# Kernel tuning notes

Hardware: AMD Instinct MI355X
Metric: run time of the kernel (lower is better)

The kernel has to match this reference:

```python
import jax, jax.numpy as jnp
import numpy as np

B, T, I, H, C = 64, 2048, 128, 256, 64


def setup_inputs() -> dict:
    key = jax.random.key(0)
    ks = jax.random.split(key, 12)
    s_ih = 1.0 / np.sqrt(H)
    inp = {
        "x": jax.random.normal(ks[0], (B, T, I), dtype=jnp.float32),
        # layer 0 GRU params (PyTorch layout: W_ih [3H, I], W_hh [3H, H])
        "W_ih0": jax.random.uniform(ks[1], (3 * H, I), minval=-s_ih, maxval=s_ih, dtype=jnp.float32),
        "W_hh0": jax.random.uniform(ks[2], (3 * H, H), minval=-s_ih, maxval=s_ih, dtype=jnp.float32),
        "b_ih0": jax.random.uniform(ks[3], (3 * H,), minval=-s_ih, maxval=s_ih, dtype=jnp.float32),
        "b_hh0": jax.random.uniform(ks[4], (3 * H,), minval=-s_ih, maxval=s_ih, dtype=jnp.float32),
        # layer 1 GRU params (input is H)
        "W_ih1": jax.random.uniform(ks[5], (3 * H, H), minval=-s_ih, maxval=s_ih, dtype=jnp.float32),
        "W_hh1": jax.random.uniform(ks[6], (3 * H, H), minval=-s_ih, maxval=s_ih, dtype=jnp.float32),
        "b_ih1": jax.random.uniform(ks[7], (3 * H,), minval=-s_ih, maxval=s_ih, dtype=jnp.float32),
        "b_hh1": jax.random.uniform(ks[8], (3 * H,), minval=-s_ih, maxval=s_ih, dtype=jnp.float32),
        # classifier head
        "fc_w": jax.random.uniform(ks[9], (C, H), minval=-s_ih, maxval=s_ih, dtype=jnp.float32),
        "fc_b": jax.random.uniform(ks[10], (C,), minval=-s_ih, maxval=s_ih, dtype=jnp.float32),
    }
    return inp


def _gru_layer(inp, W_ih, W_hh, b_ih, b_hh):
    # inp: [B, T, D_in] -> out: [B, T, H]; PyTorch GRU cell math.
    h_dim = W_hh.shape[1]
    # Precompute input-side gate pre-activations for the whole sequence (one big GEMM).
    gates_x = jnp.einsum("btd,gd->btg", inp, W_ih) + b_ih  # [B, T, 3H]

    def step(h, gx):
        gh = h @ W_hh.T + b_hh  # [B, 3H]
        xr, xz, xn = jnp.split(gx, 3, axis=-1)
        hr, hz, hn = jnp.split(gh, 3, axis=-1)
        r = jax.nn.sigmoid(xr + hr)
        z = jax.nn.sigmoid(xz + hz)
        n = jnp.tanh(xn + r * hn)
        h_new = (1.0 - z) * n + z * h
        return h_new, h_new

    h0 = jnp.zeros((inp.shape[0], h_dim), dtype=inp.dtype)
    _, out_tbh = jax.lax.scan(step, h0, jnp.swapaxes(gates_x, 0, 1))  # [T, B, H]
    return jnp.swapaxes(out_tbh, 0, 1)  # [B, T, H]


def reference(x, W_ih0, W_hh0, b_ih0, b_hh0, W_ih1, W_hh1, b_ih1, b_hh1, fc_w, fc_b):
    h = _gru_layer(x, W_ih0, W_hh0, b_ih0, b_hh0)
    h = _gru_layer(h, W_ih1, W_hh1, b_ih1, b_hh1)
    return h @ fc_w.T + fc_b  # [B, T, C]
```

## Files before the change

### kernel.cpp

```cpp
#include <hip/hip_runtime.h>

typedef _Float16 half2_t __attribute__((ext_vector_type(2)));
typedef _Float16 half8_t __attribute__((ext_vector_type(8)));
typedef float floatx4 __attribute__((ext_vector_type(4)));
typedef unsigned int u32;

#define BB 64
#define TT 2048
#define II 128
#define HH 256
#define CC 64
#define G3 (3*HH)
#define MTOT (BB*TT)

static __device__ __forceinline__ float dot2f(half2_t a, half2_t b, float c) {
#if __has_builtin(__builtin_amdgcn_fdot2)
    return __builtin_amdgcn_fdot2(a, b, c, false);
#else
    return c + (float)a[0]*(float)b[0] + (float)a[1]*(float)b[1];
#endif
}

template<typename AT, typename CT>
__global__ __launch_bounds__(256, 2)
void gemm_mfma(const AT* __restrict__ A, const float* __restrict__ W,
               const float* __restrict__ bias, CT* __restrict__ Cout,
               int M, int N, int K)
{
    __shared__ alignas(16) u32 As32[128 * 32];
    __shared__ alignas(16) u32 Bs32[64 * 32];

    const int tid  = threadIdx.x;
    const int lane = tid & 63;
    const int wave = tid >> 6;
    const int wm   = wave >> 1;
    const int wn   = wave & 1;
    const int m0   = blockIdx.y * 128;
    const int n0   = blockIdx.x * 64;
    const int lr   = lane & 15;
    const int lg   = lane >> 4;

    floatx4 acc[4][2] = {};

    for (int kc = 0; kc < K; kc += 64) {
        #pragma unroll
        for (int it = 0; it < 4; ++it) {
            const int s    = it * 256 + tid;
            const int row  = s >> 3;
            const int slot = s & 7;
            const AT* src  = A + (size_t)(m0 + row) * K + kc + slot * 8;
            half8_t v;
            if constexpr (sizeof(AT) == 2) {
                v = *reinterpret_cast<const half8_t*>(src);
            } else {
                const float4* s4 = reinterpret_cast<const float4*>(src);
                float4 lo = s4[0], hi = s4[1];
                v[0] = (_Float16)lo.x; v[1] = (_Float16)lo.y;
                v[2] = (_Float16)lo.z; v[3] = (_Float16)lo.w;
                v[4] = (_Float16)hi.x; v[5] = (_Float16)hi.y;
                v[6] = (_Float16)hi.z; v[7] = (_Float16)hi.w;
            }
            const int sw = slot ^ (row & 7);
            *reinterpret_cast<half8_t*>(&As32[row * 32 + sw * 4]) = v;
        }
        #pragma unroll
        for (int it = 0; it < 2; ++it) {
            const int s    = it * 256 + tid;
            const int row  = s >> 3;
            const int slot = s & 7;
            const float* src = W + (size_t)(n0 + row) * K + kc + slot * 8;
            const float4* s4 = reinterpret_cast<const float4*>(src);
            float4 lo = s4[0], hi = s4[1];
            half8_t v;
            v[0] = (_Float16)lo.x; v[1] = (_Float16)lo.y;
            v[2] = (_Float16)lo.z; v[3] = (_Float16)lo.w;
            v[4] = (_Float16)hi.x; v[5] = (_Float16)hi.y;
            v[6] = (_Float16)hi.z; v[7] = (_Float16)hi.w;
            const int sw = slot ^ (row & 7);
            *reinterpret_cast<half8_t*>(&Bs32[row * 32 + sw * 4]) = v;
        }
        __syncthreads();

        #pragma unroll
        for (int ks = 0; ks < 2; ++ks) {
            half8_t af[4], bf[2];
            #pragma unroll
            for (int fm = 0; fm < 4; ++fm) {
                const int row  = wm * 64 + fm * 16 + lr;
                const int slot = ks * 4 + lg;
                const int sw   = slot ^ (row & 7);
                af[fm] = *reinterpret_cast<const half8_t*>(&As32[row * 32 + sw * 4]);
            }
            #pragma unroll
            for (int fn = 0; fn < 2; ++fn) {
                const int row  = wn * 32 + fn * 16 + lr;
                const int slot = ks * 4 + lg;
                const int sw   = slot ^ (row & 7);
                bf[fn] = *reinterpret_cast<const half8_t*>(&Bs32[row * 32 + sw * 4]);
            }
            #pragma unroll
            for (int fm = 0; fm < 4; ++fm)
                #pragma unroll
                for (int fn = 0; fn < 2; ++fn)
                    acc[fm][fn] = __builtin_amdgcn_mfma_f32_16x16x32_f16(
                        af[fm], bf[fn], acc[fm][fn], 0, 0, 0);
        }
        __syncthreads();
    }

    #pragma unroll
    for (int fn = 0; fn < 2; ++fn) {
        const int n = n0 + wn * 32 + fn * 16 + lr;
        const float bv = bias[n];
        #pragma unroll
        for (int fm = 0; fm < 4; ++fm) {
            #pragma unroll
            for (int r = 0; r < 4; ++r) {
                const int m = m0 + wm * 64 + fm * 16 + lg * 4 + r;
                Cout[(size_t)m * N + n] = (CT)(acc[fm][fn][r] + bv);
            }
        }
    }
}

__global__ __launch_bounds__(512, 2)
void gru_scan(const _Float16* __restrict__ gx,
              const float* __restrict__ Whh,
              const float* __restrict__ bhh,
              _Float16* __restrict__ hout)
{
    const int b  = blockIdx.x;
    const int t  = threadIdx.x;
    const int j  = t >> 1;
    const int kh = t & 1;

    half2_t w0[64], w1[64], w2[64];
    {
        const float* p0 = Whh + (size_t)j * HH + kh * 128;
        const float* p1 = p0 + 256 * HH;
        const float* p2 = p0 + 512 * HH;
        #pragma unroll
        for (int i = 0; i < 64; ++i) {
            w0[i] = half2_t{(_Float16)p0[2*i], (_Float16)p0[2*i+1]};
            w1[i] = half2_t{(_Float16)p1[2*i], (_Float16)p1[2*i+1]};
            w2[i] = half2_t{(_Float16)p2[2*i], (_Float16)p2[2*i+1]};
        }
    }
    const float bh_r = bhh[j], bh_z = bhh[HH + j], bh_n = bhh[2*HH + j];

    __shared__ alignas(16) u32 h2[HH/2];
    if (t < HH/2) h2[t] = 0u;
    float hprev = 0.f;
    __syncthreads();

    const _Float16* g = gx + (size_t)b * TT * G3;
    u32* op = (u32*)(hout + (size_t)b * TT * HH);

    for (int step = 0; step < TT; ++step) {
        float xr = (float)g[j];
        float xz = (float)g[HH + j];
        float xn = (float)g[2*HH + j];

        const uint4* hb = (const uint4*)(h2 + kh * 64);
        float ar = 0.f, az = 0.f, an = 0.f;
        #pragma unroll
        for (int c = 0; c < 16; ++c) {
            uint4 hv = hb[c];
            half2_t ha = __builtin_bit_cast(half2_t, hv.x);
            half2_t hc = __builtin_bit_cast(half2_t, hv.y);
            half2_t hd = __builtin_bit_cast(half2_t, hv.z);
            half2_t he = __builtin_bit_cast(half2_t, hv.w);
            ar = dot2f(ha, w0[4*c+0], ar); az = dot2f(ha, w1[4*c+0], az); an = dot2f(ha, w2[4*c+0], an);
            ar = dot2f(hc, w0[4*c+1], ar); az = dot2f(hc, w1[4*c+1], az); an = dot2f(hc, w2[4*c+1], an);
            ar = dot2f(hd, w0[4*c+2], ar); az = dot2f(hd, w1[4*c+2], az); an = dot2f(hd, w2[4*c+2], an);
            ar = dot2f(he, w0[4*c+3], ar); az = dot2f(he, w1[4*c+3], az); an = dot2f(he, w2[4*c+3], an);
        }
        ar += __shfl_xor(ar, 1);
        az += __shfl_xor(az, 1);
        an += __shfl_xor(an, 1);

        const float r = 1.f / (1.f + __expf(-(xr + ar + bh_r)));
        const float z = 1.f / (1.f + __expf(-(xz + az + bh_z)));
        const float e = __expf(2.f * (xn + r * (an + bh_n)));
        const float n = 1.f - 2.f / (e + 1.f);
        const float hnew = (1.f - z) * n + z * hprev;
        hprev = hnew;

        const float hother = __shfl_xor(hnew, 2);
        __syncthreads();
        if ((t & 3) == 0) {
            half2_t hp{(_Float16)hnew, (_Float16)hother};
            const u32 pu = __builtin_bit_cast(u32, hp);
            h2[t >> 2] = pu;
            op[t >> 2] = pu;
        }
        __syncthreads();
        g  += G3;
        op += HH/2;
    }
}

extern "C" void kernel_launch(void* const* d_in, const int* in_sizes, int n_in,
                              void* d_out, int out_size, void* d_ws, size_t ws_size,
                              hipStream_t stream) {
    const float* x    = (const float*)d_in[0];
    const float* Wih0 = (const float*)d_in[1];
    const float* Whh0 = (const float*)d_in[2];
    const float* bih0 = (const float*)d_in[3];
    const float* bhh0 = (const float*)d_in[4];
    const float* Wih1 = (const float*)d_in[5];
    const float* Whh1 = (const float*)d_in[6];
    const float* bih1 = (const float*)d_in[7];
    const float* bhh1 = (const float*)d_in[8];
    const float* fcw  = (const float*)d_in[9];
    const float* fcb  = (const float*)d_in[10];
    float* out = (float*)d_out;

    _Float16* gxbuf = (_Float16*)d_ws;
    _Float16* hbuf  = (_Float16*)((char*)d_ws + (size_t)MTOT * G3 * sizeof(_Float16));

    const dim3 blk(256);
    gemm_mfma<float, _Float16><<<dim3(G3/64, MTOT/128), blk, 0, stream>>>(
        x, Wih0, bih0, gxbuf, MTOT, G3, II);
    gru_scan<<<dim3(BB), dim3(512), 0, stream>>>(gxbuf, Whh0, bhh0, hbuf);
    gemm_mfma<_Float16, _Float16><<<dim3(G3/64, MTOT/128), blk, 0, stream>>>(
        hbuf, Wih1, bih1, gxbuf, MTOT, G3, HH);
    gru_scan<<<dim3(BB), dim3(512), 0, stream>>>(gxbuf, Whh1, bhh1, hbuf);
    gemm_mfma<_Float16, float><<<dim3(CC/64, MTOT/128), blk, 0, stream>>>(
        hbuf, fcw, fcb, out, MTOT, CC, HH);
}
```

Measured before the change: 5.213 ms.

## Split GRU scan K across 4 lanes, double-buffer hidden state, prefetch gates

The recurrent scan now runs 1024 threads per batch with each hidden unit's dot product split across four lanes instead of two. This halves per-thread weight registers and the serial dot-product chain, with the partial sums reduced by DPP quad moves. The hidden state is double-buffered in shared memory, so each step needs one barrier instead of two. Next-step gate inputs are prefetched, and divisions become hardware reciprocals. The costs are more threads per block, a slightly less accurate reciprocal, and 16-bit scattered stores to output and shared memory.

```diff
diff --git a/kernel.cpp b/kernel.cpp
--- a/kernel.cpp
+++ b/kernel.cpp
@@ -19,6 +19,23 @@
 #else
     return c + (float)a[0]*(float)b[0] + (float)a[1]*(float)b[1];
 #endif
+}
+
+static __device__ __forceinline__ half2_t bch2(u32 x) {
+    return __builtin_bit_cast(half2_t, x);
+}
+
+static __device__ __forceinline__ float quad_allsum(float x) {
+    int i = __builtin_bit_cast(int, x);
+    int a = __builtin_amdgcn_mov_dpp(i, 0xB1, 0xF, 0xF, true);
+    float y = x + __builtin_bit_cast(float, a);
+    int k = __builtin_bit_cast(int, y);
+    int b = __builtin_amdgcn_mov_dpp(k, 0x4E, 0xF, 0xF, true);
+    return y + __builtin_bit_cast(float, b);
+}
+
+static __device__ __forceinline__ float fast_rcp(float x) {
+    return __builtin_amdgcn_rcpf(x);
 }
 
 template<typename AT, typename CT>
@@ -123,7 +140,7 @@
     }
 }
 
-__global__ __launch_bounds__(512, 2)
+__global__ __launch_bounds__(1024, 4)
 void gru_scan(const _Float16* __restrict__ gx,
               const float* __restrict__ Whh,
               const float* __restrict__ bhh,
@@ -131,16 +148,16 @@
 {
     const int b  = blockIdx.x;
     const int t  = threadIdx.x;
-    const int j  = t >> 1;
-    const int kh = t & 1;
-
-    half2_t w0[64], w1[64], w2[64];
+    const int j  = t >> 2;
+    const int kq = t & 3;
+
+    half2_t w0[32], w1[32], w2[32];
     {
-        const float* p0 = Whh + (size_t)j * HH + kh * 128;
+        const float* p0 = Whh + (size_t)j * HH + kq * 64;
         const float* p1 = p0 + 256 * HH;
         const float* p2 = p0 + 512 * HH;
         #pragma unroll
-        for (int i = 0; i < 64; ++i) {
+        for (int i = 0; i < 32; ++i) {
             w0[i] = half2_t{(_Float16)p0[2*i], (_Float16)p0[2*i+1]};
             w1[i] = half2_t{(_Float16)p1[2*i], (_Float16)p1[2*i+1]};
             w2[i] = half2_t{(_Float16)p2[2*i], (_Float16)p2[2*i+1]};
@@ -148,55 +165,55 @@
     }
     const float bh_r = bhh[j], bh_z = bhh[HH + j], bh_n = bhh[2*HH + j];
 
-    __shared__ alignas(16) u32 h2[HH/2];
-    if (t < HH/2) h2[t] = 0u;
+    __shared__ alignas(16) _Float16 hs[2][HH];
+    if (t < HH/2) reinterpret_cast<u32*>(hs[0])[t] = 0u;
     float hprev = 0.f;
+
+    const _Float16* gj = gx + (size_t)b * TT * G3 + j;
+    _Float16* op = hout + (size_t)b * TT * HH + j;
+
+    float xr = (float)gj[0];
+    float xz = (float)gj[HH];
+    float xn = (float)gj[2*HH];
     __syncthreads();
 
-    const _Float16* g = gx + (size_t)b * TT * G3;
-    u32* op = (u32*)(hout + (size_t)b * TT * HH);
-
     for (int step = 0; step < TT; ++step) {
-        float xr = (float)g[j];
-        float xz = (float)g[HH + j];
-        float xn = (float)g[2*HH + j];
-
-        const uint4* hb = (const uint4*)(h2 + kh * 64);
+        const _Float16* gn = gj + G3;
+        const _Float16 pxr = gn[0];
+        const _Float16 pxz = gn[HH];
+        const _Float16 pxn = gn[2*HH];
+
+        const uint4* hb = reinterpret_cast<const uint4*>(hs[step & 1] + kq * 64);
         float ar = 0.f, az = 0.f, an = 0.f;
         #pragma unroll
-        for (int c = 0; c < 16; ++c) {
-            uint4 hv = hb[c];
-            half2_t ha = __builtin_bit_cast(half2_t, hv.x);
-            half2_t hc = __builtin_bit_cast(half2_t, hv.y);
-            half2_t hd = __builtin_bit_cast(half2_t, hv.z);
-            half2_t he = __builtin_bit_cast(half2_t, hv.w);
+        for (int c = 0; c < 8; ++c) {
+            const uint4 hv = hb[c];
+            const half2_t ha = bch2(hv.x), hc = bch2(hv.y);
+            const half2_t hd = bch2(hv.z), he = bch2(hv.w);
             ar = dot2f(ha, w0[4*c+0], ar); az = dot2f(ha, w1[4*c+0], az); an = dot2f(ha, w2[4*c+0], an);
             ar = dot2f(hc, w0[4*c+1], ar); az = dot2f(hc, w1[4*c+1], az); an = dot2f(hc, w2[4*c+1], an);
             ar = dot2f(hd, w0[4*c+2], ar); az = dot2f(hd, w1[4*c+2], az); an = dot2f(hd, w2[4*c+2], an);
             ar = dot2f(he, w0[4*c+3], ar); az = dot2f(he, w1[4*c+3], az); an = dot2f(he, w2[4*c+3], an);
         }
-        ar += __shfl_xor(ar, 1);
-        az += __shfl_xor(az, 1);
-        an += __shfl_xor(an, 1);
-
-        const float r = 1.f / (1.f + __expf(-(xr + ar + bh_r)));
-        const float z = 1.f / (1.f + __expf(-(xz + az + bh_z)));
+        ar = quad_allsum(ar);
+        az = quad_allsum(az);
+        an = quad_allsum(an);
+
+        const float r = fast_rcp(1.f + __expf(-(xr + ar + bh_r)));
+        const float z = fast_rcp(1.f + __expf(-(xz + az + bh_z)));
         const float e = __expf(2.f * (xn + r * (an + bh_n)));
-        const float n = 1.f - 2.f / (e + 1.f);
-        const float hnew = (1.f - z) * n + z * hprev;
+        const float nn = 1.f - 2.f * fast_rcp(e + 1.f);
+        const float hnew = (1.f - z) * nn + z * hprev;
         hprev = hnew;
 
-        const float hother = __shfl_xor(hnew, 2);
+        if (kq == 0) {
+            hs[(step + 1) & 1][j] = (_Float16)hnew;
+            op[0] = (_Float16)hnew;
+        }
         __syncthreads();
-        if ((t & 3) == 0) {
-            half2_t hp{(_Float16)hnew, (_Float16)hother};
-            const u32 pu = __builtin_bit_cast(u32, hp);
-            h2[t >> 2] = pu;
-            op[t >> 2] = pu;
-        }
-        __syncthreads();
-        g  += G3;
-        op += HH/2;
+
+        gj = gn; op += HH;
+        xr = (float)pxr; xz = (float)pxz; xn = (float)pxn;
     }
 }
 
@@ -222,10 +239,10 @@
     const dim3 blk(256);
     gemm_mfma<float, _Float16><<<dim3(G3/64, MTOT/128), blk, 0, stream>>>(
         x, Wih0, bih0, gxbuf, MTOT, G3, II);
-    gru_scan<<<dim3(BB), dim3(512), 0, stream>>>(gxbuf, Whh0, bhh0, hbuf);
+    gru_scan<<<dim3(BB), dim3(1024), 0, stream>>>(gxbuf, Whh0, bhh0, hbuf);
     gemm_mfma<_Float16, _Float16><<<dim3(G3/64, MTOT/128), blk, 0, stream>>>(
         hbuf, Wih1, bih1, gxbuf, MTOT, G3, HH);
-    gru_scan<<<dim3(BB), dim3(512), 0, stream>>>(gxbuf, Whh1, bhh1, hbuf);
+    gru_scan<<<dim3(BB), dim3(1024), 0, stream>>>(gxbuf, Whh1, bhh1, hbuf);
     gemm_mfma<_Float16, float><<<dim3(CC/64, MTOT/128), blk, 0, stream>>>(
         hbuf, fcw, fcb, out, MTOT, CC, HH);
 }
```

Result: faster. 5.106 ms (-2.0%).

## Compute GRU recurrent matvec with MFMA and double-buffer hidden state in LDS

Applied to the files above, without the earlier changes.

The recurrent h·W_hh product in the scan kernel now runs on 16x16x32 f16 MFMA instructions, with h broadcast across the A rows and W_hh fragments held in registers. Previously it used per-thread fdot2 loops with a pair-shuffle reduction. The hidden state is double-buffered in LDS so each step needs one barrier instead of two. The next step's gate inputs are prefetched, and sigmoid/tanh use a hardware reciprocal. The trade-off is that 15 of 16 MFMA rows are wasted, only 16 lanes per wave do the gate math, and 48 half8 weight fragments per thread raise register pressure.

```diff
diff --git a/kernel.cpp b/kernel.cpp
--- a/kernel.cpp
+++ b/kernel.cpp
@@ -13,12 +13,8 @@
 #define G3 (3*HH)
 #define MTOT (BB*TT)
 
-static __device__ __forceinline__ float dot2f(half2_t a, half2_t b, float c) {
-#if __has_builtin(__builtin_amdgcn_fdot2)
-    return __builtin_amdgcn_fdot2(a, b, c, false);
-#else
-    return c + (float)a[0]*(float)b[0] + (float)a[1]*(float)b[1];
-#endif
+static __device__ __forceinline__ float fast_rcp(float x) {
+    return __builtin_amdgcn_rcpf(x);
 }
 
 template<typename AT, typename CT>
@@ -129,74 +125,106 @@
               const float* __restrict__ bhh,
               _Float16* __restrict__ hout)
 {
-    const int b  = blockIdx.x;
-    const int t  = threadIdx.x;
-    const int j  = t >> 1;
-    const int kh = t & 1;
-
-    half2_t w0[64], w1[64], w2[64];
-    {
-        const float* p0 = Whh + (size_t)j * HH + kh * 128;
-        const float* p1 = p0 + 256 * HH;
-        const float* p2 = p0 + 512 * HH;
-        #pragma unroll
-        for (int i = 0; i < 64; ++i) {
-            w0[i] = half2_t{(_Float16)p0[2*i], (_Float16)p0[2*i+1]};
-            w1[i] = half2_t{(_Float16)p1[2*i], (_Float16)p1[2*i+1]};
-            w2[i] = half2_t{(_Float16)p2[2*i], (_Float16)p2[2*i+1]};
-        }
-    }
-    const float bh_r = bhh[j], bh_z = bhh[HH + j], bh_n = bhh[2*HH + j];
-
-    __shared__ alignas(16) u32 h2[HH/2];
-    if (t < HH/2) h2[t] = 0u;
-    float hprev = 0.f;
+    const int b    = blockIdx.x;
+    const int tid  = threadIdx.x;
+    const int wv   = tid >> 6;
+    const int lane = tid & 63;
+    const int lr   = lane & 15;
+    const int lg   = lane >> 4;
+
+    half8_t wf[48];
+    #pragma unroll
+    for (int g = 0; g < 3; ++g) {
+        #pragma unroll
+        for (int p = 0; p < 2; ++p) {
+            const int row = g * 256 + wv * 32 + p * 16 + lr;
+            #pragma unroll
+            for (int kf = 0; kf < 8; ++kf) {
+                const float* src = Whh + (size_t)row * HH + kf * 32 + lg * 8;
+                const float4 lo = reinterpret_cast<const float4*>(src)[0];
+                const float4 hi = reinterpret_cast<const float4*>(src)[1];
+                half8_t v;
+                v[0] = (_Float16)lo.x; v[1] = (_Float16)lo.y;
+                v[2] = (_Float16)lo.z; v[3] = (_Float16)lo.w;
+                v[4] = (_Float16)hi.x; v[5] = (_Float16)hi.y;
+                v[6] = (_Float16)hi.z; v[7] = (_Float16)hi.w;
+                wf[(g * 2 + p) * 8 + kf] = v;
+            }
+        }
+    }
+
+    const int j0 = wv * 32 + lr;
+    float bhr[2], bhz[2], bhn[2];
+    #pragma unroll
+    for (int p = 0; p < 2; ++p) {
+        bhr[p] = bhh[j0 + p * 16];
+        bhz[p] = bhh[HH + j0 + p * 16];
+        bhn[p] = bhh[2 * HH + j0 + p * 16];
+    }
+
+    __shared__ alignas(16) _Float16 Hs[2][HH];
+    reinterpret_cast<_Float16*>(Hs)[tid] = (_Float16)0.f;
+
+    const _Float16* gp = gx + (size_t)b * TT * G3 + j0;
+    _Float16* op = hout + (size_t)b * TT * HH + j0;
+
+    _Float16 pxr0 = 0, pxz0 = 0, pxn0 = 0, pxr1 = 0, pxz1 = 0, pxn1 = 0;
+    if (lane < 16) {
+        pxr0 = gp[0];       pxr1 = gp[16];
+        pxz0 = gp[HH];      pxz1 = gp[HH + 16];
+        pxn0 = gp[2 * HH];  pxn1 = gp[2 * HH + 16];
+    }
+    float hp0 = 0.f, hp1 = 0.f;
     __syncthreads();
 
-    const _Float16* g = gx + (size_t)b * TT * G3;
-    u32* op = (u32*)(hout + (size_t)b * TT * HH);
-
-    for (int step = 0; step < TT; ++step) {
-        float xr = (float)g[j];
-        float xz = (float)g[HH + j];
-        float xn = (float)g[2*HH + j];
-
-        const uint4* hb = (const uint4*)(h2 + kh * 64);
-        float ar = 0.f, az = 0.f, an = 0.f;
-        #pragma unroll
-        for (int c = 0; c < 16; ++c) {
-            uint4 hv = hb[c];
-            half2_t ha = __builtin_bit_cast(half2_t, hv.x);
-            half2_t hc = __builtin_bit_cast(half2_t, hv.y);
-            half2_t hd = __builtin_bit_cast(half2_t, hv.z);
-            half2_t he = __builtin_bit_cast(half2_t, hv.w);
-            ar = dot2f(ha, w0[4*c+0], ar); az = dot2f(ha, w1[4*c+0], az); an = dot2f(ha, w2[4*c+0], an);
-            ar = dot2f(hc, w0[4*c+1], ar); az = dot2f(hc, w1[4*c+1], az); an = dot2f(hc, w2[4*c+1], an);
-            ar = dot2f(hd, w0[4*c+2], ar); az = dot2f(hd, w1[4*c+2], az); an = dot2f(hd, w2[4*c+2], an);
-            ar = dot2f(he, w0[4*c+3], ar); az = dot2f(he, w1[4*c+3], az); an = dot2f(he, w2[4*c+3], an);
-        }
-        ar += __shfl_xor(ar, 1);
-        az += __shfl_xor(az, 1);
-        an += __shfl_xor(an, 1);
-
-        const float r = 1.f / (1.f + __expf(-(xr + ar + bh_r)));
-        const float z = 1.f / (1.f + __expf(-(xz + az + bh_z)));
-        const float e = __expf(2.f * (xn + r * (an + bh_n)));
-        const float n = 1.f - 2.f / (e + 1.f);
-        const float hnew = (1.f - z) * n + z * hprev;
-        hprev = hnew;
-
-        const float hother = __shfl_xor(hnew, 2);
+    for (int t = 0; t < TT; ++t) {
+        const _Float16* hcur = Hs[t & 1];
+        _Float16*       hnxt = Hs[(t + 1) & 1];
+
+        floatx4 acc[6] = {};
+        #pragma unroll
+        for (int kf = 0; kf < 8; ++kf) {
+            const half8_t a = *reinterpret_cast<const half8_t*>(&hcur[kf * 32 + lg * 8]);
+            #pragma unroll
+            for (int i = 0; i < 6; ++i)
+                acc[i] = __builtin_amdgcn_mfma_f32_16x16x32_f16(
+                    a, wf[i * 8 + kf], acc[i], 0, 0, 0);
+        }
+
+        if (lane < 16) {
+            const _Float16 nxr0 = gp[G3],           nxr1 = gp[G3 + 16];
+            const _Float16 nxz0 = gp[G3 + HH],      nxz1 = gp[G3 + HH + 16];
+            const _Float16 nxn0 = gp[G3 + 2 * HH],  nxn1 = gp[G3 + 2 * HH + 16];
+
+            {
+                const float ar = acc[0][0], az = acc[2][0], an = acc[4][0];
+                const float r = fast_rcp(1.f + __expf(-((float)pxr0 + ar + bhr[0])));
+                const float z = fast_rcp(1.f + __expf(-((float)pxz0 + az + bhz[0])));
+                const float e = __expf(2.f * ((float)pxn0 + r * (an + bhn[0])));
+                const float n = 1.f - 2.f * fast_rcp(e + 1.f);
+                const float hnew = (1.f - z) * n + z * hp0;
+                hp0 = hnew;
+                const _Float16 hf = (_Float16)hnew;
+                hnxt[j0] = hf;
+                op[0] = hf;
+            }
+            {
+                const float ar = acc[1][0], az = acc[3][0], an = acc[5][0];
+                const float r = fast_rcp(1.f + __expf(-((float)pxr1 + ar + bhr[1])));
+                const float z = fast_rcp(1.f + __expf(-((float)pxz1 + az + bhz[1])));
+                const float e = __expf(2.f * ((float)pxn1 + r * (an + bhn[1])));
+                const float n = 1.f - 2.f * fast_rcp(e + 1.f);
+                const float hnew = (1.f - z) * n + z * hp1;
+                hp1 = hnew;
+                const _Float16 hf = (_Float16)hnew;
+                hnxt[j0 + 16] = hf;
+                op[16] = hf;
+            }
+            pxr0 = nxr0; pxz0 = nxz0; pxn0 = nxn0;
+            pxr1 = nxr1; pxz1 = nxz1; pxn1 = nxn1;
+        }
         __syncthreads();
-        if ((t & 3) == 0) {
-            half2_t hp{(_Float16)hnew, (_Float16)hother};
-            const u32 pu = __builtin_bit_cast(u32, hp);
-            h2[t >> 2] = pu;
-            op[t >> 2] = pu;
-        }
-        __syncthreads();
-        g  += G3;
-        op += HH/2;
+        gp += G3; op += HH;
     }
 }
 
```

Result: slower. 5.415 ms (+3.9%).

## Double-buffer GRU hidden state, prefetch gate inputs, use DPP lane exchange

Applied to the files above, without the earlier changes.

The GRU recurrence kernel now ping-pongs the shared hidden state between two buffers. This lets each timestep use a single barrier instead of two. It also loads the next timestep's input-gate values one step ahead, so their global latency overlaps the current step's dot products. Lane exchanges switch from shuffle to DPP moves and the divisions in the gates use the hardware reciprocal, both to shorten the per-step serial critical path. The prefetch reads one row past the end of each batch's gate buffer on the last step, and the reciprocal is slightly less precise than a true division.

```diff
diff --git a/kernel.cpp b/kernel.cpp
--- a/kernel.cpp
+++ b/kernel.cpp
@@ -19,6 +19,25 @@
 #else
     return c + (float)a[0]*(float)b[0] + (float)a[1]*(float)b[1];
 #endif
+}
+
+static __device__ __forceinline__ half2_t bch2(u32 x) {
+    return __builtin_bit_cast(half2_t, x);
+}
+
+static __device__ __forceinline__ float fast_rcp(float x) {
+    return __builtin_amdgcn_rcpf(x);
+}
+
+static __device__ __forceinline__ float pair_sum(float x) {
+    int i = __builtin_bit_cast(int, x);
+    int a = __builtin_amdgcn_mov_dpp(i, 0xB1, 0xF, 0xF, true);
+    return x + __builtin_bit_cast(float, a);
+}
+static __device__ __forceinline__ float dpp_xor2(float x) {
+    int i = __builtin_bit_cast(int, x);
+    int a = __builtin_amdgcn_mov_dpp(i, 0x4E, 0xF, 0xF, true);
+    return __builtin_bit_cast(float, a);
 }
 
 template<typename AT, typename CT>
@@ -123,7 +142,8 @@
     }
 }
 
-__global__ __launch_bounds__(512, 2)
+__global__ __attribute__((amdgpu_flat_work_group_size(512, 512),
+                          amdgpu_waves_per_eu(2, 2)))
 void gru_scan(const _Float16* __restrict__ gx,
               const float* __restrict__ Whh,
               const float* __restrict__ bhh,
@@ -136,67 +156,68 @@
 
     half2_t w0[64], w1[64], w2[64];
     {
-        const float* p0 = Whh + (size_t)j * HH + kh * 128;
-        const float* p1 = p0 + 256 * HH;
-        const float* p2 = p0 + 512 * HH;
+        const float2* q0 = reinterpret_cast<const float2*>(Whh + (size_t)j * HH + kh * 128);
+        const float2* q1 = q0 + 128 * HH;
+        const float2* q2 = q0 + 256 * HH;
         #pragma unroll
         for (int i = 0; i < 64; ++i) {
-            w0[i] = half2_t{(_Float16)p0[2*i], (_Float16)p0[2*i+1]};
-            w1[i] = half2_t{(_Float16)p1[2*i], (_Float16)p1[2*i+1]};
-            w2[i] = half2_t{(_Float16)p2[2*i], (_Float16)p2[2*i+1]};
+            const float2 a = q0[i], c = q1[i], d = q2[i];
+            w0[i] = half2_t{(_Float16)a.x, (_Float16)a.y};
+            w1[i] = half2_t{(_Float16)c.x, (_Float16)c.y};
+            w2[i] = half2_t{(_Float16)d.x, (_Float16)d.y};
         }
     }
     const float bh_r = bhh[j], bh_z = bhh[HH + j], bh_n = bhh[2*HH + j];
 
-    __shared__ alignas(16) u32 h2[HH/2];
-    if (t < HH/2) h2[t] = 0u;
+    __shared__ alignas(16) _Float16 Hs[2][HH];
+    reinterpret_cast<_Float16*>(Hs)[t] = (_Float16)0.f;
     float hprev = 0.f;
+
+    const _Float16* gp = gx + (size_t)b * TT * G3 + j;
+    u32* opw = (u32*)(hout + (size_t)b * TT * HH);
+
+    _Float16 pxr = gp[0], pxz = gp[HH], pxn = gp[2*HH];
     __syncthreads();
 
-    const _Float16* g = gx + (size_t)b * TT * G3;
-    u32* op = (u32*)(hout + (size_t)b * TT * HH);
-
     for (int step = 0; step < TT; ++step) {
-        float xr = (float)g[j];
-        float xz = (float)g[HH + j];
-        float xn = (float)g[2*HH + j];
-
-        const uint4* hb = (const uint4*)(h2 + kh * 64);
+        const _Float16 nxr = gp[G3];
+        const _Float16 nxz = gp[G3 + HH];
+        const _Float16 nxn = gp[G3 + 2*HH];
+
+        const uint4* hb = reinterpret_cast<const uint4*>(Hs[step & 1] + kh * 128);
         float ar = 0.f, az = 0.f, an = 0.f;
         #pragma unroll
         for (int c = 0; c < 16; ++c) {
-            uint4 hv = hb[c];
-            half2_t ha = __builtin_bit_cast(half2_t, hv.x);
-            half2_t hc = __builtin_bit_cast(half2_t, hv.y);
-            half2_t hd = __builtin_bit_cast(half2_t, hv.z);
-            half2_t he = __builtin_bit_cast(half2_t, hv.w);
+            const uint4 hv = hb[c];
+            const half2_t ha = bch2(hv.x), hc = bch2(hv.y);
+            const half2_t hd = bch2(hv.z), he = bch2(hv.w);
             ar = dot2f(ha, w0[4*c+0], ar); az = dot2f(ha, w1[4*c+0], az); an = dot2f(ha, w2[4*c+0], an);
             ar = dot2f(hc, w0[4*c+1], ar); az = dot2f(hc, w1[4*c+1], az); an = dot2f(hc, w2[4*c+1], an);
             ar = dot2f(hd, w0[4*c+2], ar); az = dot2f(hd, w1[4*c+2], az); an = dot2f(hd, w2[4*c+2], an);
             ar = dot2f(he, w0[4*c+3], ar); az = dot2f(he, w1[4*c+3], az); an = dot2f(he, w2[4*c+3], an);
         }
-        ar += __shfl_xor(ar, 1);
-        az += __shfl_xor(az, 1);
-        an += __shfl_xor(an, 1);
-
-        const float r = 1.f / (1.f + __expf(-(xr + ar + bh_r)));
-        const float z = 1.f / (1.f + __expf(-(xz + az + bh_z)));
-        const float e = __expf(2.f * (xn + r * (an + bh_n)));
-        const float n = 1.f - 2.f / (e + 1.f);
+        ar = pair_sum(ar);
+        az = pair_sum(az);
+        an = pair_sum(an);
+
+        const float r = fast_rcp(1.f + __expf(-((float)pxr + ar + bh_r)));
+        const float z = fast_rcp(1.f + __expf(-((float)pxz + az + bh_z)));
+        const float e = __expf(2.f * ((float)pxn + r * (an + bh_n)));
+        const float n = 1.f - 2.f * fast_rcp(e + 1.f);
         const float hnew = (1.f - z) * n + z * hprev;
         hprev = hnew;
 
-        const float hother = __shfl_xor(hnew, 2);
+        const float hoth = dpp_xor2(hnew);
+        if ((t & 3) == 0) {
+            const half2_t hp{(_Float16)hnew, (_Float16)hoth};
+            const u32 pu = __builtin_bit_cast(u32, hp);
+            reinterpret_cast<u32*>(Hs[(step + 1) & 1])[t >> 2] = pu;
+            opw[t >> 2] = pu;
+        }
         __syncthreads();
-        if ((t & 3) == 0) {
-            half2_t hp{(_Float16)hnew, (_Float16)hother};
-            const u32 pu = __builtin_bit_cast(u32, hp);
-            h2[t >> 2] = pu;
-            op[t >> 2] = pu;
-        }
-        __syncthreads();
-        g  += G3;
-        op += HH/2;
+
+        gp += G3; opw += HH/2;
+        pxr = nxr; pxz = nxz; pxn = nxn;
     }
 }
 
```

New measurement: 4.597 ms. -11.8%, faster.
